# Kernel optimization log

Hardware: AMD Instinct MI355X
Metric: run time of the kernel (lower is better)

The kernel has to match this reference:

```python
import jax, jax.numpy as jnp
import numpy as np

V, E = 50000, 400000
ND, ED, OUT = 128, 64, 128  # node feat, edge feat, out_dim
IN = ND + ED
NEG_SLOPE = 0.01
BN_EPS = 1e-5


def setup_inputs() -> dict:
    key = jax.random.key(0)
    ks = jax.random.split(key, 12)
    s = lambda d: 1.0 / np.sqrt(d)
    return {
        "node_feats": jax.random.normal(ks[0], (V, ND), jnp.float32),
        "edge_feats": jax.random.normal(ks[1], (E, ED), jnp.float32),
        "src": jax.random.randint(ks[2], (E,), 0, V, jnp.int32),
        "dst": jax.random.randint(ks[3], (E,), 0, V, jnp.int32),
        "W1": jax.random.uniform(ks[4], (IN, OUT), jnp.float32, -s(IN), s(IN)),
        "b1": jnp.zeros((OUT,), jnp.float32),
        "W2": jax.random.uniform(ks[5], (OUT, OUT), jnp.float32, -s(OUT), s(OUT)),
        "b2": jnp.zeros((OUT,), jnp.float32),
        "W3": jax.random.uniform(ks[6], (OUT, OUT), jnp.float32, -s(OUT), s(OUT)),
        "b3": jnp.zeros((OUT,), jnp.float32),
        "gamma": jnp.ones((OUT,), jnp.float32),
        "beta": jnp.zeros((OUT,), jnp.float32),
    }


def _lrelu(x):
    return jnp.where(x >= 0, x, NEG_SLOPE * x)


def reference(node_feats, edge_feats, src, dst, W1, b1, W2, b2, W3, b3, gamma, beta):
    # u_add_v: gather source + destination node features per edge  [E, ND]
    m = node_feats[src] + node_feats[dst]
    # concat edge feats with message: [E, ED+ND] = [E, IN]
    x = jnp.concatenate([edge_feats, m], axis=1)
    h = _lrelu(x @ W1 + b1)
    h = _lrelu(h @ W2 + b2)
    h = _lrelu(h @ W3 + b3)
    # dropout p=0 -> identity; BatchNorm1d (training mode, batch stats over edges)
    mean = jnp.mean(h, axis=0)
    var = jnp.mean((h - mean) ** 2, axis=0)  # biased variance
    return gamma * (h - mean) * jax.lax.rsqrt(var + BN_EPS) + beta
```

## Files before the change

### kernel.cpp

```cpp
#include <hip/hip_runtime.h>
#include <hip/hip_bf16.h>
#include <cstddef>

#define N_E 400000
#define N_V 50000
#define NEG_SLOPE 0.01f
#define BN_EPS 1e-5f
#define NT (N_E / 64)

typedef __attribute__((ext_vector_type(8))) short bf16x8;
typedef __attribute__((ext_vector_type(4))) float f32x4;

#define PART_OFF   0
#define SCALE_OFF  65536
#define WT_OFF     66560
#define META_END   181248
#define Y_BYTES    12800000ULL
#define H_BYTES    102400000ULL
#define OUT_BYTES  204800000ULL

#define SWX(row, chunk) ((row) * 64 + ((((chunk) ^ ((row) & 7))) << 3))
#define SWM(row, chunk) ((row) * 128 + ((((chunk) ^ ((row) & 7))) << 3))

__device__ __forceinline__ unsigned short f2bf(float f) {
  unsigned u = __builtin_bit_cast(unsigned, f);
  u += 0x7fffu + ((u >> 16) & 1u);
  return (unsigned short)(u >> 16);
}
__device__ __forceinline__ float bf2f(unsigned short s) {
  return __builtin_bit_cast(float, (unsigned)s << 16);
}
__device__ __forceinline__ float lrelu(float x) {
  return x >= 0.f ? x : NEG_SLOPE * x;
}
__device__ __forceinline__ unsigned pk2(float lo, float hi) {
  unsigned r;
  asm("v_cvt_pk_bf16_f32 %0, %1, %2" : "=v"(r) : "v"(lo), "v"(hi));
  return r;
}
__device__ __forceinline__ int addbf(int a, int b) {
  unsigned ua = (unsigned)a, ub = (unsigned)b;
  float l = __builtin_bit_cast(float, ua << 16) + __builtin_bit_cast(float, ub << 16);
  float h = __builtin_bit_cast(float, ua & 0xffff0000u) +
            __builtin_bit_cast(float, ub & 0xffff0000u);
  return (int)pk2(l, h);
}

template<bool USEWS>
__global__ __launch_bounds__(256, 4) void gnn4(
    const float* __restrict__ edgef, const int* __restrict__ srcI,
    const int* __restrict__ dstI, const short* __restrict__ ybuf,
    const float* __restrict__ b1, const float* __restrict__ b2,
    const float* __restrict__ b3, const short* __restrict__ wt,
    float* __restrict__ partials, short* __restrict__ hout,
    float* __restrict__ fout) {
  __shared__ short sX[64 * 64];
  __shared__ short sM[64 * 128];
  __shared__ short sN[64 * 128];

  const int tid = threadIdx.x;
  const int lane = tid & 63;
  const int w = tid >> 6;
  const int col = lane & 15;
  const int lq = lane >> 4;
  const int t = blockIdx.x;
  const int r4 = tid >> 2, c4 = tid & 3;

  {
    int e = t * 64 + r4;
    int si = srcI[e], di = dstI[e];
    const float4* efp = (const float4*)(edgef + (size_t)e * 64) + c4 * 4;
    float4 e0 = efp[0], e1 = efp[1], e2 = efp[2], e3 = efp[3];
    const int4* yps = (const int4*)(ybuf + (size_t)si * 128) + c4 * 4;
    const int4* ypd = (const int4*)(ybuf + (size_t)di * 128) + c4 * 4;
    int4 a0 = yps[0], a1 = yps[1], a2 = yps[2], a3 = yps[3];
    int4 d0 = ypd[0], d1 = ypd[1], d2 = ypd[2], d3 = ypd[3];
    int4 x0, x1;
    x0.x = (int)pk2(e0.x, e0.y); x0.y = (int)pk2(e0.z, e0.w);
    x0.z = (int)pk2(e1.x, e1.y); x0.w = (int)pk2(e1.z, e1.w);
    x1.x = (int)pk2(e2.x, e2.y); x1.y = (int)pk2(e2.z, e2.w);
    x1.z = (int)pk2(e3.x, e3.y); x1.w = (int)pk2(e3.z, e3.w);
    *(int4*)(sX + SWX(r4, c4 * 2)) = x0;
    *(int4*)(sX + SWX(r4, c4 * 2 + 1)) = x1;
    int4 y0, y1, y2, y3;
    y0.x = addbf(a0.x, d0.x); y0.y = addbf(a0.y, d0.y);
    y0.z = addbf(a0.z, d0.z); y0.w = addbf(a0.w, d0.w);
    y1.x = addbf(a1.x, d1.x); y1.y = addbf(a1.y, d1.y);
    y1.z = addbf(a1.z, d1.z); y1.w = addbf(a1.w, d1.w);
    y2.x = addbf(a2.x, d2.x); y2.y = addbf(a2.y, d2.y);
    y2.z = addbf(a2.z, d2.z); y2.w = addbf(a2.w, d2.w);
    y3.x = addbf(a3.x, d3.x); y3.y = addbf(a3.y, d3.y);
    y3.z = addbf(a3.z, d3.z); y3.w = addbf(a3.w, d3.w);
    *(int4*)(sM + SWM(r4, c4 * 4 + 0)) = y0;
    *(int4*)(sM + SWM(r4, c4 * 4 + 1)) = y1;
    *(int4*)(sM + SWM(r4, c4 * 4 + 2)) = y2;
    *(int4*)(sM + SWM(r4, c4 * 4 + 3)) = y3;
  }

  f32x4 acc[2][4];
  #pragma unroll
  for (int tt = 0; tt < 2; ++tt)
    #pragma unroll
    for (int et = 0; et < 4; ++et) acc[tt][et] = (f32x4){0.f, 0.f, 0.f, 0.f};
  float sE[8], sQ[8];
  #pragma unroll
  for (int i = 0; i < 8; ++i) { sE[i] = 0.f; sQ[i] = 0.f; }

  __syncthreads();

  {
    bf16x8 f1[2][2];
    #pragma unroll
    for (int tt = 0; tt < 2; ++tt)
      #pragma unroll
      for (int s = 0; s < 2; ++s)
        f1[tt][s] = *(const bf16x8*)(wt + ((((w * 2 + tt) * 2 + s) << 9) + lane * 8));
    float4 bbA = *(const float4*)(b1 + (w * 2 + 0) * 16 + lq * 4);
    float4 bbB = *(const float4*)(b1 + (w * 2 + 1) * 16 + lq * 4);
    #pragma unroll
    for (int et = 0; et < 4; ++et) {
      const int row = et * 16 + col;
      #pragma unroll
      for (int s = 0; s < 2; ++s) {
        bf16x8 b = *(const bf16x8*)(sX + SWX(row, lq + s * 4));
        acc[0][et] = __builtin_amdgcn_mfma_f32_16x16x32_bf16(f1[0][s], b, acc[0][et], 0, 0, 0);
        acc[1][et] = __builtin_amdgcn_mfma_f32_16x16x32_bf16(f1[1][s], b, acc[1][et], 0, 0, 0);
      }
    }
    #pragma unroll
    for (int tt = 0; tt < 2; ++tt) {
      const int f0 = (w * 2 + tt) * 16 + lq * 4;
      const int ch = f0 >> 3, sub = f0 & 7;
      float4 bb = tt ? bbB : bbA;
      #pragma unroll
      for (int et = 0; et < 4; ++et) {
        const int edge = et * 16 + col;
        short4 q = *(const short4*)(sM + SWM(edge, ch) + sub);
        f32x4 a = acc[tt][et];
        float v0 = lrelu(a[0] + bb.x + bf2f((unsigned short)q.x));
        float v1 = lrelu(a[1] + bb.y + bf2f((unsigned short)q.y));
        float v2 = lrelu(a[2] + bb.z + bf2f((unsigned short)q.z));
        float v3 = lrelu(a[3] + bb.w + bf2f((unsigned short)q.w));
        *(int2*)(sN + SWM(edge, ch) + sub) = make_int2((int)pk2(v0, v1), (int)pk2(v2, v3));
        acc[tt][et] = (f32x4){0.f, 0.f, 0.f, 0.f};
      }
    }
  }
  __syncthreads();

  {
    bf16x8 f2[2][4];
    #pragma unroll
    for (int tt = 0; tt < 2; ++tt)
      #pragma unroll
      for (int s = 0; s < 4; ++s)
        f2[tt][s] = *(const bf16x8*)(wt + 24576 + ((((w * 2 + tt) * 4 + s) << 9) + lane * 8));
    float4 bbA = *(const float4*)(b2 + (w * 2 + 0) * 16 + lq * 4);
    float4 bbB = *(const float4*)(b2 + (w * 2 + 1) * 16 + lq * 4);
    #pragma unroll
    for (int et = 0; et < 4; ++et) {
      const int row = et * 16 + col;
      #pragma unroll
      for (int s = 0; s < 4; ++s) {
        bf16x8 b = *(const bf16x8*)(sN + SWM(row, lq + s * 4));
        acc[0][et] = __builtin_amdgcn_mfma_f32_16x16x32_bf16(f2[0][s], b, acc[0][et], 0, 0, 0);
        acc[1][et] = __builtin_amdgcn_mfma_f32_16x16x32_bf16(f2[1][s], b, acc[1][et], 0, 0, 0);
      }
    }
    #pragma unroll
    for (int tt = 0; tt < 2; ++tt) {
      const int f0 = (w * 2 + tt) * 16 + lq * 4;
      const int ch = f0 >> 3, sub = f0 & 7;
      float4 bb = tt ? bbB : bbA;
      #pragma unroll
      for (int et = 0; et < 4; ++et) {
        const int edge = et * 16 + col;
        f32x4 a = acc[tt][et];
        float v0 = lrelu(a[0] + bb.x), v1 = lrelu(a[1] + bb.y);
        float v2 = lrelu(a[2] + bb.z), v3 = lrelu(a[3] + bb.w);
        *(int2*)(sM + SWM(edge, ch) + sub) = make_int2((int)pk2(v0, v1), (int)pk2(v2, v3));
        acc[tt][et] = (f32x4){0.f, 0.f, 0.f, 0.f};
      }
    }
  }
  __syncthreads();

  {
    bf16x8 f3[2][4];
    #pragma unroll
    for (int tt = 0; tt < 2; ++tt)
      #pragma unroll
      for (int s = 0; s < 4; ++s)
        f3[tt][s] = *(const bf16x8*)(wt + 40960 + ((((w * 2 + tt) * 4 + s) << 9) + lane * 8));
    float4 bbA = *(const float4*)(b3 + (w * 2 + 0) * 16 + lq * 4);
    float4 bbB = *(const float4*)(b3 + (w * 2 + 1) * 16 + lq * 4);
    #pragma unroll
    for (int et = 0; et < 4; ++et) {
      const int row = et * 16 + col;
      #pragma unroll
      for (int s = 0; s < 4; ++s) {
        bf16x8 b = *(const bf16x8*)(sM + SWM(row, lq + s * 4));
        acc[0][et] = __builtin_amdgcn_mfma_f32_16x16x32_bf16(f3[0][s], b, acc[0][et], 0, 0, 0);
        acc[1][et] = __builtin_amdgcn_mfma_f32_16x16x32_bf16(f3[1][s], b, acc[1][et], 0, 0, 0);
      }
    }
    #pragma unroll
    for (int tt = 0; tt < 2; ++tt) {
      const int f0 = (w * 2 + tt) * 16 + lq * 4;
      const int ch = f0 >> 3, sub = f0 & 7;
      float4 bb = tt ? bbB : bbA;
      #pragma unroll
      for (int et = 0; et < 4; ++et) {
        const int edge = et * 16 + col;
        f32x4 a = acc[tt][et];
        float v0 = lrelu(a[0] + bb.x), v1 = lrelu(a[1] + bb.y);
        float v2 = lrelu(a[2] + bb.z), v3 = lrelu(a[3] + bb.w);
        sE[tt * 4 + 0] += v0; sQ[tt * 4 + 0] += v0 * v0;
        sE[tt * 4 + 1] += v1; sQ[tt * 4 + 1] += v1 * v1;
        sE[tt * 4 + 2] += v2; sQ[tt * 4 + 2] += v2 * v2;
        sE[tt * 4 + 3] += v3; sQ[tt * 4 + 3] += v3 * v3;
        *(int2*)(sN + SWM(edge, ch) + sub) = make_int2((int)pk2(v0, v1), (int)pk2(v2, v3));
      }
    }
  }
  __syncthreads();

  if (USEWS) {
    int4* dst = (int4*)(hout + (size_t)t * 8192);
    #pragma unroll
    for (int j = 0; j < 4; ++j)
      dst[r4 * 16 + c4 * 4 + j] = *(const int4*)(sN + SWM(r4, c4 * 4 + j));
  } else {
    float4* dst = (float4*)(fout + (size_t)t * 8192);
    #pragma unroll
    for (int j = 0; j < 4; ++j) {
      int4 tv = *(const int4*)(sN + SWM(r4, c4 * 4 + j));
      float4 o0, o1;
      o0.x = bf2f((unsigned short)((unsigned)tv.x & 0xffffu));
      o0.y = bf2f((unsigned short)((unsigned)tv.x >> 16));
      o0.z = bf2f((unsigned short)((unsigned)tv.y & 0xffffu));
      o0.w = bf2f((unsigned short)((unsigned)tv.y >> 16));
      o1.x = bf2f((unsigned short)((unsigned)tv.z & 0xffffu));
      o1.y = bf2f((unsigned short)((unsigned)tv.z >> 16));
      o1.z = bf2f((unsigned short)((unsigned)tv.w & 0xffffu));
      o1.w = bf2f((unsigned short)((unsigned)tv.w >> 16));
      dst[r4 * 32 + c4 * 8 + j * 2] = o0;
      dst[r4 * 32 + c4 * 8 + j * 2 + 1] = o1;
    }
  }

  #pragma unroll
  for (int m = 1; m <= 8; m <<= 1) {
    #pragma unroll
    for (int i = 0; i < 8; ++i) {
      sE[i] += __shfl_xor(sE[i], m, 64);
      sQ[i] += __shfl_xor(sQ[i], m, 64);
    }
  }
  if (col == 0) {
    float* pp = partials + (t & 63) * 256;
    #pragma unroll
    for (int tt = 0; tt < 2; ++tt) {
      const int f0 = (w * 2 + tt) * 16 + lq * 4;
      #pragma unroll
      for (int i = 0; i < 4; ++i) {
        atomicAdd(&pp[f0 + i], sE[tt * 4 + i]);
        atomicAdd(&pp[128 + f0 + i], sQ[tt * 4 + i]);
      }
    }
  }
}

__global__ __launch_bounds__(256) void nodeK(const float* __restrict__ nodef,
                                             const short* __restrict__ wt,
                                             short* __restrict__ y) {
  __shared__ short sN[64 * 136];
  const int tid = threadIdx.x;
  const int lane = tid & 63;
  const int w = tid >> 6;
  const int n0 = blockIdx.x * 64;
  const int r = tid >> 2, p4 = tid & 3;
  {
    int v = n0 + r;
    int vc = v < N_V ? v : N_V - 1;
    const float4* np = (const float4*)(nodef + (size_t)vc * 128) + p4 * 8;
    #pragma unroll
    for (int j = 0; j < 8; ++j) {
      float4 a = np[j];
      *(int2*)(sN + r * 136 + p4 * 32 + j * 4) =
          make_int2((int)pk2(a.x, a.y), (int)pk2(a.z, a.w));
    }
  }
  __syncthreads();
  const short* wb = wt + 8192;
  bf16x8 fr[8];
  #pragma unroll
  for (int nt = 0; nt < 2; ++nt)
    #pragma unroll
    for (int s = 0; s < 4; ++s)
      fr[nt * 4 + s] = *(const bf16x8*)(wb + ((((w * 2 + nt) * 4 + s) << 9) + lane * 8));
  f32x4 acc[8];
  #pragma unroll
  for (int i = 0; i < 8; ++i) acc[i] = (f32x4){0.f, 0.f, 0.f, 0.f};
  const int col = lane & 15;
  const int kb = (lane >> 4) * 8;
  #pragma unroll
  for (int et = 0; et < 4; ++et) {
    const short* bp = sN + (et * 16 + col) * 136 + kb;
    #pragma unroll
    for (int s = 0; s < 4; ++s) {
      bf16x8 b = *(const bf16x8*)(bp + s * 32);
      acc[0 + et] = __builtin_amdgcn_mfma_f32_16x16x32_bf16(fr[s], b, acc[0 + et], 0, 0, 0);
      acc[4 + et] = __builtin_amdgcn_mfma_f32_16x16x32_bf16(fr[4 + s], b, acc[4 + et], 0, 0, 0);
    }
  }
  __syncthreads();
  {
    const int fb = (lane >> 4) * 4;
    #pragma unroll
    for (int nt = 0; nt < 2; ++nt) {
      const int f0 = w * 32 + nt * 16 + fb;
      #pragma unroll
      for (int et = 0; et < 4; ++et) {
        f32x4 a = acc[nt * 4 + et];
        *(int2*)(sN + (et * 16 + col) * 136 + f0) =
            make_int2((int)pk2(a[0], a[1]), (int)pk2(a[2], a[3]));
      }
    }
  }
  __syncthreads();
  if (n0 + r < N_V) {
    #pragma unroll
    for (int j = 0; j < 4; ++j) {
      int4 tv = *(const int4*)(sN + r * 136 + p4 * 32 + j * 8);
      *(int4*)(y + (size_t)(n0 + r) * 128 + p4 * 32 + j * 8) = tv;
    }
  }
}

__global__ __launch_bounds__(256) void prepK(const float* __restrict__ W1,
                                             const float* __restrict__ W2,
                                             const float* __restrict__ W3,
                                             short* __restrict__ wt,
                                             float* __restrict__ partials) {
  int b = blockIdx.x, t = threadIdx.x;
  if (b < 64) { partials[b * 256 + t] = 0.f; return; }
  int g = (b - 64) * 256 + t;
  for (int fi = g; fi < 57344; fi += 32 * 256) {
    float val;
    if (fi < 8192) {
      int c = fi >> 9, r = fi & 511;
      int l = r >> 3, j = r & 7;
      int tt = c >> 1, s = c & 1;
      int n = tt * 16 + (l & 15);
      int k = s * 32 + (l >> 4) * 8 + j;
      val = W1[k * 128 + n];
    } else if (fi < 24576) {
      int f2 = fi - 8192;
      int c = f2 >> 9, r = f2 & 511;
      int l = r >> 3, j = r & 7;
      int tt = c >> 2, s = c & 3;
      int n = tt * 16 + (l & 15);
      int k = s * 32 + (l >> 4) * 8 + j;
      val = W1[(64 + k) * 128 + n];
    } else if (fi < 40960) {
      int f2 = fi - 24576;
      int c = f2 >> 9, r = f2 & 511;
      int l = r >> 3, j = r & 7;
      int tt = c >> 2, s = c & 3;
      int n = tt * 16 + (l & 15);
      int k = s * 32 + (l >> 4) * 8 + j;
      val = W2[k * 128 + n];
    } else {
      int f3 = fi - 40960;
      int c = f3 >> 9, r = f3 & 511;
      int l = r >> 3, j = r & 7;
      int tt = c >> 2, s = c & 3;
      int n = tt * 16 + (l & 15);
      int k = s * 32 + (l >> 4) * 8 + j;
      val = W3[k * 128 + n];
    }
    wt[fi] = (short)f2bf(val);
  }
}

__global__ __launch_bounds__(256) void statsK(const float* __restrict__ partials,
                                              const float* __restrict__ gamma,
                                              const float* __restrict__ beta,
                                              float* __restrict__ scsh) {
  __shared__ float tmp[256];
  int t = threadIdx.x;
  float a = 0.f;
  #pragma unroll 8
  for (int r = 0; r < 64; ++r) a += partials[r * 256 + t];
  tmp[t] = a;
  __syncthreads();
  if (t < 128) {
    float S = tmp[t], S2 = tmp[t + 128];
    float mean = S / (float)N_E;
    float var = S2 / (float)N_E - mean * mean;
    float inv = rsqrtf(var + BN_EPS);
    float sc = gamma[t] * inv;
    scsh[t] = sc;
    scsh[t + 128] = beta[t] - mean * sc;
  }
}

template<bool USEWS>
__global__ __launch_bounds__(256) void applyK(const short* __restrict__ h,
                                              const float* __restrict__ scsh,
                                              float* out) {
  const int TOT4 = N_E * 128 / 4;
  int j0 = blockIdx.x * 256 + threadIdx.x;
  int c4 = j0 & 31;
  float4 sc = *(const float4*)(scsh + c4 * 4);
  float4 sh = *(const float4*)(scsh + 128 + c4 * 4);
  int stride = gridDim.x * 256;
  for (int j = j0; j < TOT4; j += stride) {
    float4 v;
    if (USEWS) {
      short4 s = *(const short4*)(h + (size_t)j * 4);
      v.x = bf2f((unsigned short)s.x) * sc.x + sh.x;
      v.y = bf2f((unsigned short)s.y) * sc.y + sh.y;
      v.z = bf2f((unsigned short)s.z) * sc.z + sh.z;
      v.w = bf2f((unsigned short)s.w) * sc.w + sh.w;
    } else {
      float4 hv = ((const float4*)out)[j];
      v.x = hv.x * sc.x + sh.x;
      v.y = hv.y * sc.y + sh.y;
      v.z = hv.z * sc.z + sh.z;
      v.w = hv.w * sc.w + sh.w;
    }
    ((float4*)out)[j] = v;
  }
}

extern "C" void kernel_launch(void* const* d_in, const int* in_sizes, int n_in,
                              void* d_out, int out_size, void* d_ws, size_t ws_size,
                              hipStream_t stream) {
  const float* nodef = (const float*)d_in[0];
  const float* edgef = (const float*)d_in[1];
  const int* srcI = (const int*)d_in[2];
  const int* dstI = (const int*)d_in[3];
  const float* W1 = (const float*)d_in[4];
  const float* b1 = (const float*)d_in[5];
  const float* W2 = (const float*)d_in[6];
  const float* b2 = (const float*)d_in[7];
  const float* W3 = (const float*)d_in[8];
  const float* b3 = (const float*)d_in[9];
  const float* gamma = (const float*)d_in[10];
  const float* beta = (const float*)d_in[11];
  float* out = (float*)d_out;
  char* ws = (char*)d_ws;

  float* partials = (float*)(ws + PART_OFF);
  float* scsh = (float*)(ws + SCALE_OFF);
  short* wt = (short*)(ws + WT_OFF);
  short* ybuf;
  short* h = nullptr;
  bool usews;
  if (ws_size >= (size_t)META_END + Y_BYTES + H_BYTES) {
    ybuf = (short*)(ws + META_END);
    h = (short*)(ws + META_END + Y_BYTES);
    usews = true;
  } else if (ws_size >= (size_t)META_END + H_BYTES) {
    h = (short*)(ws + META_END);
    ybuf = (short*)((char*)d_out + OUT_BYTES - Y_BYTES);
    usews = true;
  } else {
    ybuf = (short*)(ws + META_END);
    usews = false;
  }

  prepK<<<96, 256, 0, stream>>>(W1, W2, W3, wt, partials);
  nodeK<<<782, 256, 0, stream>>>(nodef, wt, ybuf);
  if (usews) {
    gnn4<true><<<NT, 256, 0, stream>>>(edgef, srcI, dstI, ybuf, b1, b2, b3,
                                       wt, partials, h, out);
  } else {
    gnn4<false><<<NT, 256, 0, stream>>>(edgef, srcI, dstI, ybuf, b1, b2, b3,
                                        wt, partials, h, out);
  }
  statsK<<<1, 256, 0, stream>>>(partials, gamma, beta, scsh);
  if (usews) {
    applyK<true><<<2048, 256, 0, stream>>>(h, scsh, out);
  } else {
    applyK<false><<<2048, 256, 0, stream>>>(h, scsh, out);
  }
}
```

Baseline: 184.3 us.

## Process two edge tiles per block with software-prefetched gathers overlapping MLP

Each block now handles two 64-edge tiles. The second tile's edge features and node-message gathers are loaded into registers while the first tile's layer-1 MFMA runs, then written to rotated shared buffers between layers. The final layer writes results straight to global memory instead of staging them through shared memory, and the per-block atomic stats count is halved. This trades higher register pressure and half as many blocks (less parallelism) for hiding gather latency behind compute.

```diff
diff --git a/kernel.cpp b/kernel.cpp
--- a/kernel.cpp
+++ b/kernel.cpp
@@ -46,8 +46,170 @@
   return (int)pk2(l, h);
 }
 
+template<bool USEWS, bool PF>
+__device__ __forceinline__ void doTile(
+    int t, int tn,
+    const float* __restrict__ edgef, const int* __restrict__ srcI,
+    const int* __restrict__ dstI, const short* __restrict__ ybuf,
+    const float* __restrict__ b1, const float* __restrict__ b2,
+    const float* __restrict__ b3, const short* __restrict__ wt,
+    short* __restrict__ hout, float* __restrict__ fout,
+    short* sX, short* sY, short* sZ,
+    f32x4 (&acc)[2][4], float (&sE)[8], float (&sQv)[8],
+    int lane, int w, int col, int lq, int r4, int c4) {
+  int4 xa, xb;
+  int4 a0, a1, a2, a3, d0, d1, d2, d3;
+  if (PF) {
+    int e = tn * 64 + r4;
+    int si = srcI[e], di = dstI[e];
+    const float4* efp = (const float4*)(edgef + (size_t)e * 64) + c4 * 4;
+    float4 e0 = efp[0], e1 = efp[1], e2 = efp[2], e3 = efp[3];
+    xa.x = (int)pk2(e0.x, e0.y); xa.y = (int)pk2(e0.z, e0.w);
+    xa.z = (int)pk2(e1.x, e1.y); xa.w = (int)pk2(e1.z, e1.w);
+    xb.x = (int)pk2(e2.x, e2.y); xb.y = (int)pk2(e2.z, e2.w);
+    xb.z = (int)pk2(e3.x, e3.y); xb.w = (int)pk2(e3.z, e3.w);
+    const int4* yps = (const int4*)(ybuf + (size_t)si * 128) + c4 * 4;
+    const int4* ypd = (const int4*)(ybuf + (size_t)di * 128) + c4 * 4;
+    a0 = yps[0]; a1 = yps[1]; a2 = yps[2]; a3 = yps[3];
+    d0 = ypd[0]; d1 = ypd[1]; d2 = ypd[2]; d3 = ypd[3];
+  }
+  {
+    bf16x8 f1[2][2];
+    #pragma unroll
+    for (int tt = 0; tt < 2; ++tt)
+      #pragma unroll
+      for (int s = 0; s < 2; ++s)
+        f1[tt][s] = *(const bf16x8*)(wt + ((((w * 2 + tt) * 2 + s) << 9) + lane * 8));
+    #pragma unroll
+    for (int et = 0; et < 4; ++et) {
+      const int row = et * 16 + col;
+      #pragma unroll
+      for (int s = 0; s < 2; ++s) {
+        bf16x8 b = *(const bf16x8*)(sX + SWX(row, lq + s * 4));
+        acc[0][et] = __builtin_amdgcn_mfma_f32_16x16x32_bf16(f1[0][s], b, acc[0][et], 0, 0, 0);
+        acc[1][et] = __builtin_amdgcn_mfma_f32_16x16x32_bf16(f1[1][s], b, acc[1][et], 0, 0, 0);
+      }
+    }
+    #pragma unroll
+    for (int tt = 0; tt < 2; ++tt) {
+      const int f0 = (w * 2 + tt) * 16 + lq * 4;
+      const int ch = f0 >> 3, sub = f0 & 7;
+      float4 bb = *(const float4*)(b1 + f0);
+      #pragma unroll
+      for (int et = 0; et < 4; ++et) {
+        const int edge = et * 16 + col;
+        short4 q = *(const short4*)(sY + SWM(edge, ch) + sub);
+        f32x4 a = acc[tt][et];
+        float v0 = lrelu(a[0] + bb.x + bf2f((unsigned short)q.x));
+        float v1 = lrelu(a[1] + bb.y + bf2f((unsigned short)q.y));
+        float v2 = lrelu(a[2] + bb.z + bf2f((unsigned short)q.z));
+        float v3 = lrelu(a[3] + bb.w + bf2f((unsigned short)q.w));
+        *(int2*)(sZ + SWM(edge, ch) + sub) = make_int2((int)pk2(v0, v1), (int)pk2(v2, v3));
+        acc[tt][et] = (f32x4){0.f, 0.f, 0.f, 0.f};
+      }
+    }
+  }
+  __syncthreads();
+  int4 y0, y1, y2, y3;
+  if (PF) {
+    *(int4*)(sX + SWX(r4, c4 * 2)) = xa;
+    *(int4*)(sX + SWX(r4, c4 * 2 + 1)) = xb;
+    y0.x = addbf(a0.x, d0.x); y0.y = addbf(a0.y, d0.y);
+    y0.z = addbf(a0.z, d0.z); y0.w = addbf(a0.w, d0.w);
+    y1.x = addbf(a1.x, d1.x); y1.y = addbf(a1.y, d1.y);
+    y1.z = addbf(a1.z, d1.z); y1.w = addbf(a1.w, d1.w);
+    y2.x = addbf(a2.x, d2.x); y2.y = addbf(a2.y, d2.y);
+    y2.z = addbf(a2.z, d2.z); y2.w = addbf(a2.w, d2.w);
+    y3.x = addbf(a3.x, d3.x); y3.y = addbf(a3.y, d3.y);
+    y3.z = addbf(a3.z, d3.z); y3.w = addbf(a3.w, d3.w);
+  }
+  {
+    bf16x8 f2[2][4];
+    #pragma unroll
+    for (int tt = 0; tt < 2; ++tt)
+      #pragma unroll
+      for (int s = 0; s < 4; ++s)
+        f2[tt][s] = *(const bf16x8*)(wt + 24576 + ((((w * 2 + tt) * 4 + s) << 9) + lane * 8));
+    #pragma unroll
+    for (int et = 0; et < 4; ++et) {
+      const int row = et * 16 + col;
+      #pragma unroll
+      for (int s = 0; s < 4; ++s) {
+        bf16x8 b = *(const bf16x8*)(sZ + SWM(row, lq + s * 4));
+        acc[0][et] = __builtin_amdgcn_mfma_f32_16x16x32_bf16(f2[0][s], b, acc[0][et], 0, 0, 0);
+        acc[1][et] = __builtin_amdgcn_mfma_f32_16x16x32_bf16(f2[1][s], b, acc[1][et], 0, 0, 0);
+      }
+    }
+    #pragma unroll
+    for (int tt = 0; tt < 2; ++tt) {
+      const int f0 = (w * 2 + tt) * 16 + lq * 4;
+      const int ch = f0 >> 3, sub = f0 & 7;
+      float4 bb = *(const float4*)(b2 + f0);
+      #pragma unroll
+      for (int et = 0; et < 4; ++et) {
+        const int edge = et * 16 + col;
+        f32x4 a = acc[tt][et];
+        float v0 = lrelu(a[0] + bb.x), v1 = lrelu(a[1] + bb.y);
+        float v2 = lrelu(a[2] + bb.z), v3 = lrelu(a[3] + bb.w);
+        *(int2*)(sY + SWM(edge, ch) + sub) = make_int2((int)pk2(v0, v1), (int)pk2(v2, v3));
+        acc[tt][et] = (f32x4){0.f, 0.f, 0.f, 0.f};
+      }
+    }
+  }
+  __syncthreads();
+  if (PF) {
+    *(int4*)(sZ + SWM(r4, c4 * 4 + 0)) = y0;
+    *(int4*)(sZ + SWM(r4, c4 * 4 + 1)) = y1;
+    *(int4*)(sZ + SWM(r4, c4 * 4 + 2)) = y2;
+    *(int4*)(sZ + SWM(r4, c4 * 4 + 3)) = y3;
+  }
+  {
+    bf16x8 f3[2][4];
+    #pragma unroll
+    for (int tt = 0; tt < 2; ++tt)
+      #pragma unroll
+      for (int s = 0; s < 4; ++s)
+        f3[tt][s] = *(const bf16x8*)(wt + 40960 + ((((w * 2 + tt) * 4 + s) << 9) + lane * 8));
+    #pragma unroll
+    for (int et = 0; et < 4; ++et) {
+      const int row = et * 16 + col;
+      #pragma unroll
+      for (int s = 0; s < 4; ++s) {
+        bf16x8 b = *(const bf16x8*)(sY + SWM(row, lq + s * 4));
+        acc[0][et] = __builtin_amdgcn_mfma_f32_16x16x32_bf16(f3[0][s], b, acc[0][et], 0, 0, 0);
+        acc[1][et] = __builtin_amdgcn_mfma_f32_16x16x32_bf16(f3[1][s], b, acc[1][et], 0, 0, 0);
+      }
+    }
+    const size_t ebase = (size_t)t * 64;
+    #pragma unroll
+    for (int tt = 0; tt < 2; ++tt) {
+      const int f0 = (w * 2 + tt) * 16 + lq * 4;
+      float4 bb = *(const float4*)(b3 + f0);
+      #pragma unroll
+      for (int et = 0; et < 4; ++et) {
+        const int edge = et * 16 + col;
+        f32x4 a = acc[tt][et];
+        float v0 = lrelu(a[0] + bb.x), v1 = lrelu(a[1] + bb.y);
+        float v2 = lrelu(a[2] + bb.z), v3 = lrelu(a[3] + bb.w);
+        sE[tt * 4 + 0] += v0; sQv[tt * 4 + 0] += v0 * v0;
+        sE[tt * 4 + 1] += v1; sQv[tt * 4 + 1] += v1 * v1;
+        sE[tt * 4 + 2] += v2; sQv[tt * 4 + 2] += v2 * v2;
+        sE[tt * 4 + 3] += v3; sQv[tt * 4 + 3] += v3 * v3;
+        if (USEWS) {
+          *(int2*)(hout + (ebase + edge) * 128 + f0) =
+              make_int2((int)pk2(v0, v1), (int)pk2(v2, v3));
+        } else {
+          *(float4*)(fout + (ebase + edge) * 128 + f0) = make_float4(v0, v1, v2, v3);
+        }
+        acc[tt][et] = (f32x4){0.f, 0.f, 0.f, 0.f};
+      }
+    }
+  }
+  __syncthreads();
+}
+
 template<bool USEWS>
-__global__ __launch_bounds__(256, 4) void gnn4(
+__global__ __launch_bounds__(256, 4) void gnn5(
     const float* __restrict__ edgef, const int* __restrict__ srcI,
     const int* __restrict__ dstI, const short* __restrict__ ybuf,
     const float* __restrict__ b1, const float* __restrict__ b2,
@@ -55,19 +217,19 @@
     float* __restrict__ partials, short* __restrict__ hout,
     float* __restrict__ fout) {
   __shared__ short sX[64 * 64];
-  __shared__ short sM[64 * 128];
-  __shared__ short sN[64 * 128];
+  __shared__ short sP[64 * 128];
+  __shared__ short sQ[64 * 128];
 
   const int tid = threadIdx.x;
   const int lane = tid & 63;
   const int w = tid >> 6;
   const int col = lane & 15;
   const int lq = lane >> 4;
-  const int t = blockIdx.x;
+  const int tA = blockIdx.x * 2, tB = tA + 1;
   const int r4 = tid >> 2, c4 = tid & 3;
 
   {
-    int e = t * 64 + r4;
+    int e = tA * 64 + r4;
     int si = srcI[e], di = dstI[e];
     const float4* efp = (const float4*)(edgef + (size_t)e * 64) + c4 * 4;
     float4 e0 = efp[0], e1 = efp[1], e2 = efp[2], e3 = efp[3];
@@ -91,10 +253,10 @@
     y2.z = addbf(a2.z, d2.z); y2.w = addbf(a2.w, d2.w);
     y3.x = addbf(a3.x, d3.x); y3.y = addbf(a3.y, d3.y);
     y3.z = addbf(a3.z, d3.z); y3.w = addbf(a3.w, d3.w);
-    *(int4*)(sM + SWM(r4, c4 * 4 + 0)) = y0;
-    *(int4*)(sM + SWM(r4, c4 * 4 + 1)) = y1;
-    *(int4*)(sM + SWM(r4, c4 * 4 + 2)) = y2;
-    *(int4*)(sM + SWM(r4, c4 * 4 + 3)) = y3;
+    *(int4*)(sP + SWM(r4, c4 * 4 + 0)) = y0;
+    *(int4*)(sP + SWM(r4, c4 * 4 + 1)) = y1;
+    *(int4*)(sP + SWM(r4, c4 * 4 + 2)) = y2;
+    *(int4*)(sP + SWM(r4, c4 * 4 + 3)) = y3;
   }
 
   f32x4 acc[2][4];
@@ -102,170 +264,36 @@
   for (int tt = 0; tt < 2; ++tt)
     #pragma unroll
     for (int et = 0; et < 4; ++et) acc[tt][et] = (f32x4){0.f, 0.f, 0.f, 0.f};
-  float sE[8], sQ[8];
+  float sE[8], sQv[8];
   #pragma unroll
-  for (int i = 0; i < 8; ++i) { sE[i] = 0.f; sQ[i] = 0.f; }
-
-  __syncthreads();
-
-  {
-    bf16x8 f1[2][2];
-    #pragma unroll
-    for (int tt = 0; tt < 2; ++tt)
-      #pragma unroll
-      for (int s = 0; s < 2; ++s)
-        f1[tt][s] = *(const bf16x8*)(wt + ((((w * 2 + tt) * 2 + s) << 9) + lane * 8));
-    float4 bbA = *(const float4*)(b1 + (w * 2 + 0) * 16 + lq * 4);
-    float4 bbB = *(const float4*)(b1 + (w * 2 + 1) * 16 + lq * 4);
-    #pragma unroll
-    for (int et = 0; et < 4; ++et) {
-      const int row = et * 16 + col;
-      #pragma unroll
-      for (int s = 0; s < 2; ++s) {
-        bf16x8 b = *(const bf16x8*)(sX + SWX(row, lq + s * 4));
-        acc[0][et] = __builtin_amdgcn_mfma_f32_16x16x32_bf16(f1[0][s], b, acc[0][et], 0, 0, 0);
-        acc[1][et] = __builtin_amdgcn_mfma_f32_16x16x32_bf16(f1[1][s], b, acc[1][et], 0, 0, 0);
-      }
-    }
+  for (int i = 0; i < 8; ++i) { sE[i] = 0.f; sQv[i] = 0.f; }
+
+  __syncthreads();
+
+  doTile<USEWS, true>(tA, tB, edgef, srcI, dstI, ybuf, b1, b2, b3, wt,
+                      hout, fout, sX, sP, sQ, acc, sE, sQv,
+                      lane, w, col, lq, r4, c4);
+  doTile<USEWS, false>(tB, 0, edgef, srcI, dstI, ybuf, b1, b2, b3, wt,
+                       hout, fout, sX, sQ, sP, acc, sE, sQv,
+                       lane, w, col, lq, r4, c4);
+
+  #pragma unroll
+  for (int m = 1; m <= 8; m <<= 1) {
+    #pragma unroll
+    for (int i = 0; i < 8; ++i) {
+      sE[i] += __shfl_xor(sE[i], m, 64);
+      sQv[i] += __shfl_xor(sQv[i], m, 64);
+    }
+  }
+  if (col == 0) {
+    float* pp = partials + (blockIdx.x & 63) * 256;
     #pragma unroll
     for (int tt = 0; tt < 2; ++tt) {
       const int f0 = (w * 2 + tt) * 16 + lq * 4;
-      const int ch = f0 >> 3, sub = f0 & 7;
-      float4 bb = tt ? bbB : bbA;
-      #pragma unroll
-      for (int et = 0; et < 4; ++et) {
-        const int edge = et * 16 + col;
-        short4 q = *(const short4*)(sM + SWM(edge, ch) + sub);
-        f32x4 a = acc[tt][et];
-        float v0 = lrelu(a[0] + bb.x + bf2f((unsigned short)q.x));
-        float v1 = lrelu(a[1] + bb.y + bf2f((unsigned short)q.y));
-        float v2 = lrelu(a[2] + bb.z + bf2f((unsigned short)q.z));
-        float v3 = lrelu(a[3] + bb.w + bf2f((unsigned short)q.w));
-        *(int2*)(sN + SWM(edge, ch) + sub) = make_int2((int)pk2(v0, v1), (int)pk2(v2, v3));
-        acc[tt][et] = (f32x4){0.f, 0.f, 0.f, 0.f};
-      }
-    }
-  }
-  __syncthreads();
-
-  {
-    bf16x8 f2[2][4];
-    #pragma unroll
-    for (int tt = 0; tt < 2; ++tt)
-      #pragma unroll
-      for (int s = 0; s < 4; ++s)
-        f2[tt][s] = *(const bf16x8*)(wt + 24576 + ((((w * 2 + tt) * 4 + s) << 9) + lane * 8));
-    float4 bbA = *(const float4*)(b2 + (w * 2 + 0) * 16 + lq * 4);
-    float4 bbB = *(const float4*)(b2 + (w * 2 + 1) * 16 + lq * 4);
-    #pragma unroll
-    for (int et = 0; et < 4; ++et) {
-      const int row = et * 16 + col;
-      #pragma unroll
-      for (int s = 0; s < 4; ++s) {
-        bf16x8 b = *(const bf16x8*)(sN + SWM(row, lq + s * 4));
-        acc[0][et] = __builtin_amdgcn_mfma_f32_16x16x32_bf16(f2[0][s], b, acc[0][et], 0, 0, 0);
-        acc[1][et] = __builtin_amdgcn_mfma_f32_16x16x32_bf16(f2[1][s], b, acc[1][et], 0, 0, 0);
-      }
-    }
-    #pragma unroll
-    for (int tt = 0; tt < 2; ++tt) {
-      const int f0 = (w * 2 + tt) * 16 + lq * 4;
-      const int ch = f0 >> 3, sub = f0 & 7;
-      float4 bb = tt ? bbB : bbA;
-      #pragma unroll
-      for (int et = 0; et < 4; ++et) {
-        const int edge = et * 16 + col;
-        f32x4 a = acc[tt][et];
-        float v0 = lrelu(a[0] + bb.x), v1 = lrelu(a[1] + bb.y);
-        float v2 = lrelu(a[2] + bb.z), v3 = lrelu(a[3] + bb.w);
-        *(int2*)(sM + SWM(edge, ch) + sub) = make_int2((int)pk2(v0, v1), (int)pk2(v2, v3));
-        acc[tt][et] = (f32x4){0.f, 0.f, 0.f, 0.f};
-      }
-    }
-  }
-  __syncthreads();
-
-  {
-    bf16x8 f3[2][4];
-    #pragma unroll
-    for (int tt = 0; tt < 2; ++tt)
-      #pragma unroll
-      for (int s = 0; s < 4; ++s)
-        f3[tt][s] = *(const bf16x8*)(wt + 40960 + ((((w * 2 + tt) * 4 + s) << 9) + lane * 8));
-    float4 bbA = *(const float4*)(b3 + (w * 2 + 0) * 16 + lq * 4);
-    float4 bbB = *(const float4*)(b3 + (w * 2 + 1) * 16 + lq * 4);
-    #pragma unroll
-    for (int et = 0; et < 4; ++et) {
-      const int row = et * 16 + col;
-      #pragma unroll
-      for (int s = 0; s < 4; ++s) {
-        bf16x8 b = *(const bf16x8*)(sM + SWM(row, lq + s * 4));
-        acc[0][et] = __builtin_amdgcn_mfma_f32_16x16x32_bf16(f3[0][s], b, acc[0][et], 0, 0, 0);
-        acc[1][et] = __builtin_amdgcn_mfma_f32_16x16x32_bf16(f3[1][s], b, acc[1][et], 0, 0, 0);
-      }
-    }
-    #pragma unroll
-    for (int tt = 0; tt < 2; ++tt) {
-      const int f0 = (w * 2 + tt) * 16 + lq * 4;
-      const int ch = f0 >> 3, sub = f0 & 7;
-      float4 bb = tt ? bbB : bbA;
-      #pragma unroll
-      for (int et = 0; et < 4; ++et) {
-        const int edge = et * 16 + col;
-        f32x4 a = acc[tt][et];
-        float v0 = lrelu(a[0] + bb.x), v1 = lrelu(a[1] + bb.y);
-        float v2 = lrelu(a[2] + bb.z), v3 = lrelu(a[3] + bb.w);
-        sE[tt * 4 + 0] += v0; sQ[tt * 4 + 0] += v0 * v0;
-        sE[tt * 4 + 1] += v1; sQ[tt * 4 + 1] += v1 * v1;
-        sE[tt * 4 + 2] += v2; sQ[tt * 4 + 2] += v2 * v2;
-        sE[tt * 4 + 3] += v3; sQ[tt * 4 + 3] += v3 * v3;
-        *(int2*)(sN + SWM(edge, ch) + sub) = make_int2((int)pk2(v0, v1), (int)pk2(v2, v3));
-      }
-    }
-  }
-  __syncthreads();
-
-  if (USEWS) {
-    int4* dst = (int4*)(hout + (size_t)t * 8192);
-    #pragma unroll
-    for (int j = 0; j < 4; ++j)
-      dst[r4 * 16 + c4 * 4 + j] = *(const int4*)(sN + SWM(r4, c4 * 4 + j));
-  } else {
-    float4* dst = (float4*)(fout + (size_t)t * 8192);
-    #pragma unroll
-    for (int j = 0; j < 4; ++j) {
-      int4 tv = *(const int4*)(sN + SWM(r4, c4 * 4 + j));
-      float4 o0, o1;
-      o0.x = bf2f((unsigned short)((unsigned)tv.x & 0xffffu));
-      o0.y = bf2f((unsigned short)((unsigned)tv.x >> 16));
-      o0.z = bf2f((unsigned short)((unsigned)tv.y & 0xffffu));
-      o0.w = bf2f((unsigned short)((unsigned)tv.y >> 16));
-      o1.x = bf2f((unsigned short)((unsigned)tv.z & 0xffffu));
-      o1.y = bf2f((unsigned short)((unsigned)tv.z >> 16));
-      o1.z = bf2f((unsigned short)((unsigned)tv.w & 0xffffu));
-      o1.w = bf2f((unsigned short)((unsigned)tv.w >> 16));
-      dst[r4 * 32 + c4 * 8 + j * 2] = o0;
-      dst[r4 * 32 + c4 * 8 + j * 2 + 1] = o1;
-    }
-  }
-
-  #pragma unroll
-  for (int m = 1; m <= 8; m <<= 1) {
-    #pragma unroll
-    for (int i = 0; i < 8; ++i) {
-      sE[i] += __shfl_xor(sE[i], m, 64);
-      sQ[i] += __shfl_xor(sQ[i], m, 64);
-    }
-  }
-  if (col == 0) {
-    float* pp = partials + (t & 63) * 256;
-    #pragma unroll
-    for (int tt = 0; tt < 2; ++tt) {
-      const int f0 = (w * 2 + tt) * 16 + lq * 4;
       #pragma unroll
       for (int i = 0; i < 4; ++i) {
         atomicAdd(&pp[f0 + i], sE[tt * 4 + i]);
-        atomicAdd(&pp[128 + f0 + i], sQ[tt * 4 + i]);
+        atomicAdd(&pp[128 + f0 + i], sQv[tt * 4 + i]);
       }
     }
   }
@@ -475,11 +503,11 @@
   prepK<<<96, 256, 0, stream>>>(W1, W2, W3, wt, partials);
   nodeK<<<782, 256, 0, stream>>>(nodef, wt, ybuf);
   if (usews) {
-    gnn4<true><<<NT, 256, 0, stream>>>(edgef, srcI, dstI, ybuf, b1, b2, b3,
-                                       wt, partials, h, out);
+    gnn5<true><<<NT / 2, 256, 0, stream>>>(edgef, srcI, dstI, ybuf, b1, b2, b3,
+                                           wt, partials, h, out);
   } else {
-    gnn4<false><<<NT, 256, 0, stream>>>(edgef, srcI, dstI, ybuf, b1, b2, b3,
-                                        wt, partials, h, out);
+    gnn5<false><<<NT / 2, 256, 0, stream>>>(edgef, srcI, dstI, ybuf, b1, b2, b3,
+                                            wt, partials, h, out);
   }
   statsK<<<1, 256, 0, stream>>>(partials, gamma, beta, scsh);
   if (usews) {
```

New measurement: 182.3 us. About the same (-1.1%).

## Use 8 waves per edge tile and write final layer output directly to global

Applied to the files above, without the earlier changes.

The fused edge MLP kernel now runs 512 threads per 64-edge tile, so each wave computes one 16-feature column block instead of two. This halves per-wave accumulators and weight fragments, cutting register pressure and raising the number of waves in flight. The last layer also stores results straight from registers to global memory, dropping one LDS staging round and a barrier. The cost is scattered 8-byte (bf16) or 16-byte (fp32) stores instead of coalesced 16-byte row copies, plus more waves per block competing at barriers.

```diff
diff --git a/kernel.cpp b/kernel.cpp
--- a/kernel.cpp
+++ b/kernel.cpp
@@ -47,7 +47,7 @@
 }
 
 template<bool USEWS>
-__global__ __launch_bounds__(256, 4) void gnn4(
+__global__ __launch_bounds__(512, 8) void gnn6(
     const float* __restrict__ edgef, const int* __restrict__ srcI,
     const int* __restrict__ dstI, const short* __restrict__ ybuf,
     const float* __restrict__ b1, const float* __restrict__ b2,
@@ -55,8 +55,8 @@
     float* __restrict__ partials, short* __restrict__ hout,
     float* __restrict__ fout) {
   __shared__ short sX[64 * 64];
-  __shared__ short sM[64 * 128];
-  __shared__ short sN[64 * 128];
+  __shared__ short sY[64 * 128];
+  __shared__ short sZ[64 * 128];
 
   const int tid = threadIdx.x;
   const int lane = tid & 63;
@@ -64,209 +64,145 @@
   const int col = lane & 15;
   const int lq = lane >> 4;
   const int t = blockIdx.x;
-  const int r4 = tid >> 2, c4 = tid & 3;
-
-  {
-    int e = t * 64 + r4;
+  const int r8 = tid >> 3, c8 = tid & 7;
+  const int f0 = w * 16 + lq * 4;
+  const int ch = f0 >> 3, sub = f0 & 7;
+
+  {
+    int e = t * 64 + r8;
     int si = srcI[e], di = dstI[e];
-    const float4* efp = (const float4*)(edgef + (size_t)e * 64) + c4 * 4;
-    float4 e0 = efp[0], e1 = efp[1], e2 = efp[2], e3 = efp[3];
-    const int4* yps = (const int4*)(ybuf + (size_t)si * 128) + c4 * 4;
-    const int4* ypd = (const int4*)(ybuf + (size_t)di * 128) + c4 * 4;
-    int4 a0 = yps[0], a1 = yps[1], a2 = yps[2], a3 = yps[3];
-    int4 d0 = ypd[0], d1 = ypd[1], d2 = ypd[2], d3 = ypd[3];
-    int4 x0, x1;
-    x0.x = (int)pk2(e0.x, e0.y); x0.y = (int)pk2(e0.z, e0.w);
-    x0.z = (int)pk2(e1.x, e1.y); x0.w = (int)pk2(e1.z, e1.w);
-    x1.x = (int)pk2(e2.x, e2.y); x1.y = (int)pk2(e2.z, e2.w);
-    x1.z = (int)pk2(e3.x, e3.y); x1.w = (int)pk2(e3.z, e3.w);
-    *(int4*)(sX + SWX(r4, c4 * 2)) = x0;
-    *(int4*)(sX + SWX(r4, c4 * 2 + 1)) = x1;
-    int4 y0, y1, y2, y3;
+    const float4* efp = (const float4*)(edgef + (size_t)e * 64) + c8 * 2;
+    float4 e0 = efp[0], e1 = efp[1];
+    const int4* yps = (const int4*)(ybuf + (size_t)si * 128) + c8 * 2;
+    const int4* ypd = (const int4*)(ybuf + (size_t)di * 128) + c8 * 2;
+    int4 a0 = yps[0], a1 = yps[1];
+    int4 d0 = ypd[0], d1 = ypd[1];
+    int4 x;
+    x.x = (int)pk2(e0.x, e0.y); x.y = (int)pk2(e0.z, e0.w);
+    x.z = (int)pk2(e1.x, e1.y); x.w = (int)pk2(e1.z, e1.w);
+    *(int4*)(sX + SWX(r8, c8)) = x;
+    int4 y0, y1;
     y0.x = addbf(a0.x, d0.x); y0.y = addbf(a0.y, d0.y);
     y0.z = addbf(a0.z, d0.z); y0.w = addbf(a0.w, d0.w);
     y1.x = addbf(a1.x, d1.x); y1.y = addbf(a1.y, d1.y);
     y1.z = addbf(a1.z, d1.z); y1.w = addbf(a1.w, d1.w);
-    y2.x = addbf(a2.x, d2.x); y2.y = addbf(a2.y, d2.y);
-    y2.z = addbf(a2.z, d2.z); y2.w = addbf(a2.w, d2.w);
-    y3.x = addbf(a3.x, d3.x); y3.y = addbf(a3.y, d3.y);
-    y3.z = addbf(a3.z, d3.z); y3.w = addbf(a3.w, d3.w);
-    *(int4*)(sM + SWM(r4, c4 * 4 + 0)) = y0;
-    *(int4*)(sM + SWM(r4, c4 * 4 + 1)) = y1;
-    *(int4*)(sM + SWM(r4, c4 * 4 + 2)) = y2;
-    *(int4*)(sM + SWM(r4, c4 * 4 + 3)) = y3;
-  }
-
-  f32x4 acc[2][4];
+    *(int4*)(sY + SWM(r8, c8 * 2)) = y0;
+    *(int4*)(sY + SWM(r8, c8 * 2 + 1)) = y1;
+  }
+
+  f32x4 acc[4];
   #pragma unroll
-  for (int tt = 0; tt < 2; ++tt)
-    #pragma unroll
-    for (int et = 0; et < 4; ++et) acc[tt][et] = (f32x4){0.f, 0.f, 0.f, 0.f};
-  float sE[8], sQ[8];
-  #pragma unroll
-  for (int i = 0; i < 8; ++i) { sE[i] = 0.f; sQ[i] = 0.f; }
-
-  __syncthreads();
-
-  {
-    bf16x8 f1[2][2];
-    #pragma unroll
-    for (int tt = 0; tt < 2; ++tt)
-      #pragma unroll
-      for (int s = 0; s < 2; ++s)
-        f1[tt][s] = *(const bf16x8*)(wt + ((((w * 2 + tt) * 2 + s) << 9) + lane * 8));
-    float4 bbA = *(const float4*)(b1 + (w * 2 + 0) * 16 + lq * 4);
-    float4 bbB = *(const float4*)(b1 + (w * 2 + 1) * 16 + lq * 4);
+  for (int i = 0; i < 4; ++i) acc[i] = (f32x4){0.f, 0.f, 0.f, 0.f};
+  float sE[4] = {0.f, 0.f, 0.f, 0.f}, sQv[4] = {0.f, 0.f, 0.f, 0.f};
+
+  __syncthreads();
+
+  {
+    bf16x8 f1[2];
+    #pragma unroll
+    for (int s = 0; s < 2; ++s)
+      f1[s] = *(const bf16x8*)(wt + (((w * 2 + s) << 9) + lane * 8));
     #pragma unroll
     for (int et = 0; et < 4; ++et) {
       const int row = et * 16 + col;
       #pragma unroll
       for (int s = 0; s < 2; ++s) {
         bf16x8 b = *(const bf16x8*)(sX + SWX(row, lq + s * 4));
-        acc[0][et] = __builtin_amdgcn_mfma_f32_16x16x32_bf16(f1[0][s], b, acc[0][et], 0, 0, 0);
-        acc[1][et] = __builtin_amdgcn_mfma_f32_16x16x32_bf16(f1[1][s], b, acc[1][et], 0, 0, 0);
+        acc[et] = __builtin_amdgcn_mfma_f32_16x16x32_bf16(f1[s], b, acc[et], 0, 0, 0);
       }
     }
-    #pragma unroll
-    for (int tt = 0; tt < 2; ++tt) {
-      const int f0 = (w * 2 + tt) * 16 + lq * 4;
-      const int ch = f0 >> 3, sub = f0 & 7;
-      float4 bb = tt ? bbB : bbA;
-      #pragma unroll
-      for (int et = 0; et < 4; ++et) {
-        const int edge = et * 16 + col;
-        short4 q = *(const short4*)(sM + SWM(edge, ch) + sub);
-        f32x4 a = acc[tt][et];
-        float v0 = lrelu(a[0] + bb.x + bf2f((unsigned short)q.x));
-        float v1 = lrelu(a[1] + bb.y + bf2f((unsigned short)q.y));
-        float v2 = lrelu(a[2] + bb.z + bf2f((unsigned short)q.z));
-        float v3 = lrelu(a[3] + bb.w + bf2f((unsigned short)q.w));
-        *(int2*)(sN + SWM(edge, ch) + sub) = make_int2((int)pk2(v0, v1), (int)pk2(v2, v3));
-        acc[tt][et] = (f32x4){0.f, 0.f, 0.f, 0.f};
-      }
-    }
-  }
-  __syncthreads();
-
-  {
-    bf16x8 f2[2][4];
-    #pragma unroll
-    for (int tt = 0; tt < 2; ++tt)
-      #pragma unroll
-      for (int s = 0; s < 4; ++s)
-        f2[tt][s] = *(const bf16x8*)(wt + 24576 + ((((w * 2 + tt) * 4 + s) << 9) + lane * 8));
-    float4 bbA = *(const float4*)(b2 + (w * 2 + 0) * 16 + lq * 4);
-    float4 bbB = *(const float4*)(b2 + (w * 2 + 1) * 16 + lq * 4);
+    float4 bb = *(const float4*)(b1 + f0);
+    #pragma unroll
+    for (int et = 0; et < 4; ++et) {
+      const int edge = et * 16 + col;
+      short4 q = *(const short4*)(sY + SWM(edge, ch) + sub);
+      f32x4 a = acc[et];
+      float v0 = lrelu(a[0] + bb.x + bf2f((unsigned short)q.x));
+      float v1 = lrelu(a[1] + bb.y + bf2f((unsigned short)q.y));
+      float v2 = lrelu(a[2] + bb.z + bf2f((unsigned short)q.z));
+      float v3 = lrelu(a[3] + bb.w + bf2f((unsigned short)q.w));
+      *(int2*)(sZ + SWM(edge, ch) + sub) = make_int2((int)pk2(v0, v1), (int)pk2(v2, v3));
+      acc[et] = (f32x4){0.f, 0.f, 0.f, 0.f};
+    }
+  }
+  __syncthreads();
+
+  {
+    bf16x8 f2[4];
+    #pragma unroll
+    for (int s = 0; s < 4; ++s)
+      f2[s] = *(const bf16x8*)(wt + 24576 + (((w * 4 + s) << 9) + lane * 8));
     #pragma unroll
     for (int et = 0; et < 4; ++et) {
       const int row = et * 16 + col;
       #pragma unroll
       for (int s = 0; s < 4; ++s) {
-        bf16x8 b = *(const bf16x8*)(sN + SWM(row, lq + s * 4));
-        acc[0][et] = __builtin_amdgcn_mfma_f32_16x16x32_bf16(f2[0][s], b, acc[0][et], 0, 0, 0);
-        acc[1][et] = __builtin_amdgcn_mfma_f32_16x16x32_bf16(f2[1][s], b, acc[1][et], 0, 0, 0);
+        bf16x8 b = *(const bf16x8*)(sZ + SWM(row, lq + s * 4));
+        acc[et] = __builtin_amdgcn_mfma_f32_16x16x32_bf16(f2[s], b, acc[et], 0, 0, 0);
       }
     }
-    #pragma unroll
-    for (int tt = 0; tt < 2; ++tt) {
-      const int f0 = (w * 2 + tt) * 16 + lq * 4;
-      const int ch = f0 >> 3, sub = f0 & 7;
-      float4 bb = tt ? bbB : bbA;
-      #pragma unroll
-      for (int et = 0; et < 4; ++et) {
-        const int edge = et * 16 + col;
-        f32x4 a = acc[tt][et];
-        float v0 = lrelu(a[0] + bb.x), v1 = lrelu(a[1] + bb.y);
-        float v2 = lrelu(a[2] + bb.z), v3 = lrelu(a[3] + bb.w);
-        *(int2*)(sM + SWM(edge, ch) + sub) = make_int2((int)pk2(v0, v1), (int)pk2(v2, v3));
-        acc[tt][et] = (f32x4){0.f, 0.f, 0.f, 0.f};
-      }
-    }
-  }
-  __syncthreads();
-
-  {
-    bf16x8 f3[2][4];
-    #pragma unroll
-    for (int tt = 0; tt < 2; ++tt)
-      #pragma unroll
-      for (int s = 0; s < 4; ++s)
-        f3[tt][s] = *(const bf16x8*)(wt + 40960 + ((((w * 2 + tt) * 4 + s) << 9) + lane * 8));
-    float4 bbA = *(const float4*)(b3 + (w * 2 + 0) * 16 + lq * 4);
-    float4 bbB = *(const float4*)(b3 + (w * 2 + 1) * 16 + lq * 4);
+    float4 bb = *(const float4*)(b2 + f0);
+    #pragma unroll
+    for (int et = 0; et < 4; ++et) {
+      const int edge = et * 16 + col;
+      f32x4 a = acc[et];
+      float v0 = lrelu(a[0] + bb.x), v1 = lrelu(a[1] + bb.y);
+      float v2 = lrelu(a[2] + bb.z), v3 = lrelu(a[3] + bb.w);
+      *(int2*)(sY + SWM(edge, ch) + sub) = make_int2((int)pk2(v0, v1), (int)pk2(v2, v3));
+      acc[et] = (f32x4){0.f, 0.f, 0.f, 0.f};
+    }
+  }
+  __syncthreads();
+
+  {
+    bf16x8 f3[4];
+    #pragma unroll
+    for (int s = 0; s < 4; ++s)
+      f3[s] = *(const bf16x8*)(wt + 40960 + (((w * 4 + s) << 9) + lane * 8));
     #pragma unroll
     for (int et = 0; et < 4; ++et) {
       const int row = et * 16 + col;
       #pragma unroll
       for (int s = 0; s < 4; ++s) {
-        bf16x8 b = *(const bf16x8*)(sM + SWM(row, lq + s * 4));
-        acc[0][et] = __builtin_amdgcn_mfma_f32_16x16x32_bf16(f3[0][s], b, acc[0][et], 0, 0, 0);
-        acc[1][et] = __builtin_amdgcn_mfma_f32_16x16x32_bf16(f3[1][s], b, acc[1][et], 0, 0, 0);
+        bf16x8 b = *(const bf16x8*)(sY + SWM(row, lq + s * 4));
+        acc[et] = __builtin_amdgcn_mfma_f32_16x16x32_bf16(f3[s], b, acc[et], 0, 0, 0);
       }
     }
-    #pragma unroll
-    for (int tt = 0; tt < 2; ++tt) {
-      const int f0 = (w * 2 + tt) * 16 + lq * 4;
-      const int ch = f0 >> 3, sub = f0 & 7;
-      float4 bb = tt ? bbB : bbA;
-      #pragma unroll
-      for (int et = 0; et < 4; ++et) {
-        const int edge = et * 16 + col;
-        f32x4 a = acc[tt][et];
-        float v0 = lrelu(a[0] + bb.x), v1 = lrelu(a[1] + bb.y);
-        float v2 = lrelu(a[2] + bb.z), v3 = lrelu(a[3] + bb.w);
-        sE[tt * 4 + 0] += v0; sQ[tt * 4 + 0] += v0 * v0;
-        sE[tt * 4 + 1] += v1; sQ[tt * 4 + 1] += v1 * v1;
-        sE[tt * 4 + 2] += v2; sQ[tt * 4 + 2] += v2 * v2;
-        sE[tt * 4 + 3] += v3; sQ[tt * 4 + 3] += v3 * v3;
-        *(int2*)(sN + SWM(edge, ch) + sub) = make_int2((int)pk2(v0, v1), (int)pk2(v2, v3));
+    float4 bb = *(const float4*)(b3 + f0);
+    const size_t ebase = (size_t)t * 64;
+    #pragma unroll
+    for (int et = 0; et < 4; ++et) {
+      const int edge = et * 16 + col;
+      f32x4 a = acc[et];
+      float v0 = lrelu(a[0] + bb.x), v1 = lrelu(a[1] + bb.y);
+      float v2 = lrelu(a[2] + bb.z), v3 = lrelu(a[3] + bb.w);
+      sE[0] += v0; sQv[0] += v0 * v0;
+      sE[1] += v1; sQv[1] += v1 * v1;
+      sE[2] += v2; sQv[2] += v2 * v2;
+      sE[3] += v3; sQv[3] += v3 * v3;
+      if (USEWS) {
+        *(int2*)(hout + (ebase + edge) * 128 + f0) =
+            make_int2((int)pk2(v0, v1), (int)pk2(v2, v3));
+      } else {
+        *(float4*)(fout + (ebase + edge) * 128 + f0) = make_float4(v0, v1, v2, v3);
       }
-    }
-  }
-  __syncthreads();
-
-  if (USEWS) {
-    int4* dst = (int4*)(hout + (size_t)t * 8192);
-    #pragma unroll
-    for (int j = 0; j < 4; ++j)
-      dst[r4 * 16 + c4 * 4 + j] = *(const int4*)(sN + SWM(r4, c4 * 4 + j));
-  } else {
-    float4* dst = (float4*)(fout + (size_t)t * 8192);
-    #pragma unroll
-    for (int j = 0; j < 4; ++j) {
-      int4 tv = *(const int4*)(sN + SWM(r4, c4 * 4 + j));
-      float4 o0, o1;
-      o0.x = bf2f((unsigned short)((unsigned)tv.x & 0xffffu));
-      o0.y = bf2f((unsigned short)((unsigned)tv.x >> 16));
-      o0.z = bf2f((unsigned short)((unsigned)tv.y & 0xffffu));
-      o0.w = bf2f((unsigned short)((unsigned)tv.y >> 16));
-      o1.x = bf2f((unsigned short)((unsigned)tv.z & 0xffffu));
-      o1.y = bf2f((unsigned short)((unsigned)tv.z >> 16));
-      o1.z = bf2f((unsigned short)((unsigned)tv.w & 0xffffu));
-      o1.w = bf2f((unsigned short)((unsigned)tv.w >> 16));
-      dst[r4 * 32 + c4 * 8 + j * 2] = o0;
-      dst[r4 * 32 + c4 * 8 + j * 2 + 1] = o1;
     }
   }
 
   #pragma unroll
   for (int m = 1; m <= 8; m <<= 1) {
     #pragma unroll
-    for (int i = 0; i < 8; ++i) {
+    for (int i = 0; i < 4; ++i) {
       sE[i] += __shfl_xor(sE[i], m, 64);
-      sQ[i] += __shfl_xor(sQ[i], m, 64);
+      sQv[i] += __shfl_xor(sQv[i], m, 64);
     }
   }
   if (col == 0) {
     float* pp = partials + (t & 63) * 256;
     #pragma unroll
-    for (int tt = 0; tt < 2; ++tt) {
-      const int f0 = (w * 2 + tt) * 16 + lq * 4;
-      #pragma unroll
-      for (int i = 0; i < 4; ++i) {
-        atomicAdd(&pp[f0 + i], sE[tt * 4 + i]);
-        atomicAdd(&pp[128 + f0 + i], sQ[tt * 4 + i]);
-      }
+    for (int i = 0; i < 4; ++i) {
+      atomicAdd(&pp[f0 + i], sE[i]);
+      atomicAdd(&pp[128 + f0 + i], sQv[i]);
     }
   }
 }
@@ -475,10 +411,10 @@
   prepK<<<96, 256, 0, stream>>>(W1, W2, W3, wt, partials);
   nodeK<<<782, 256, 0, stream>>>(nodef, wt, ybuf);
   if (usews) {
-    gnn4<true><<<NT, 256, 0, stream>>>(edgef, srcI, dstI, ybuf, b1, b2, b3,
+    gnn6<true><<<NT, 512, 0, stream>>>(edgef, srcI, dstI, ybuf, b1, b2, b3,
                                        wt, partials, h, out);
   } else {
-    gnn4<false><<<NT, 256, 0, stream>>>(edgef, srcI, dstI, ybuf, b1, b2, b3,
+    gnn6<false><<<NT, 512, 0, stream>>>(edgef, srcI, dstI, ybuf, b1, b2, b3,
                                         wt, partials, h, out);
   }
   statsK<<<1, 256, 0, stream>>>(partials, gamma, beta, scsh);
```

New measurement: 185.6 us. No clear change (+0.7%).
